# Optimization experiments

Measured on AMD Instinct MI355X. Metric: run time of the kernel, lower is better.

## Reference

```python
import jax, jax.numpy as jnp
import numpy as np

B, T, C = 4, 2048, 1024
H = 16
D = C // H  # 64

def setup_inputs() -> dict:
    key = jax.random.key(0)
    k1, k2, k3, k4, k5 = jax.random.split(key, 5)
    s = 0.02
    return {
        "x": jax.random.normal(k1, (B, T, C), dtype=jnp.float32),
        "Wqkv": jax.random.normal(k2, (C, 3 * C), dtype=jnp.float32) * s,
        "bqkv": jnp.zeros((3 * C,), dtype=jnp.float32),
        "Wout": jax.random.normal(k3, (C, C), dtype=jnp.float32) * s,
        "bout": jnp.zeros((C,), dtype=jnp.float32),
    }

def reference(x, Wqkv, bqkv, Wout, bout):
    b, t, c = x.shape
    scale = D ** -0.5
    qkv = x @ Wqkv + bqkv                      # [B,T,3C]
    qkv = qkv.reshape(b, t, 3, H, D)
    q = qkv[:, :, 0].transpose(0, 2, 1, 3)     # [B,H,T,D]
    k = qkv[:, :, 1].transpose(0, 2, 1, 3)
    v = qkv[:, :, 2].transpose(0, 2, 1, 3)
    att = jnp.einsum('bhqd,bhkd->bhqk', q, k) * scale
    causal = jnp.tril(jnp.ones((t, t), dtype=bool))
    att = jnp.where(causal, att, -jnp.inf)
    att = jax.nn.softmax(att, axis=-1)
    y = jnp.einsum('bhqk,bhkd->bhqd', att, v)  # [B,H,T,D]
    y = y.transpose(0, 2, 1, 3).reshape(b, t, c)
    return y @ Wout + bout
```

## Files before the change

kernel.cpp:

```cpp
#include <hip/hip_runtime.h>
#include <hip/hip_bf16.h>


using f32x4 = __attribute__((ext_vector_type(4))) float;
using s16x8 = __attribute__((ext_vector_type(8))) short;
using s16x4 = __attribute__((ext_vector_type(4))) short;

#define MFMA16(a, b, c) __builtin_amdgcn_mfma_f32_16x16x32_bf16(a, b, c, 0, 0, 0)

__device__ __forceinline__ unsigned short f2bf(float f) {
    unsigned u = __builtin_bit_cast(unsigned, f);
    u += 0x7fffu + ((u >> 16) & 1u);
    return (unsigned short)(u >> 16);
}

__device__ __forceinline__ void gl_lds16(const void* g, void* l) {
    __builtin_amdgcn_global_load_lds(
        (const __attribute__((address_space(1))) void*)g,
        (__attribute__((address_space(3))) void*)l, 16, 0, 0);
}

#define VMCNT(N) asm volatile("s_waitcnt vmcnt(" #N ")" ::: "memory")
#define RBAR()   __builtin_amdgcn_s_barrier()

__global__ __launch_bounds__(256) void cvt_x(const float* __restrict__ x,
                                             unsigned short* __restrict__ xb, int n4) {
    int i = blockIdx.x * 256 + threadIdx.x;
    if (i < n4) {
        f32x4 v = ((const f32x4*)x)[i];
        s16x4 o;
        o[0] = (short)f2bf(v[0]); o[1] = (short)f2bf(v[1]);
        o[2] = (short)f2bf(v[2]); o[3] = (short)f2bf(v[3]);
        ((s16x4*)xb)[i] = o;
    }
}

__global__ __launch_bounds__(256) void cvt_tr(const float* __restrict__ W,
                                              unsigned short* __restrict__ Wt,
                                              int R, int Cc) {
    __shared__ unsigned short tile[64][72];
    const int r0 = blockIdx.x * 64, c0 = blockIdx.y * 64;
    const int tid = threadIdx.x;
    const int r = tid >> 4, c4 = (tid & 15) * 4;
#pragma unroll
    for (int i = 0; i < 4; ++i) {
        f32x4 v = *(const f32x4*)(W + (size_t)(r0 + r + i * 16) * Cc + c0 + c4);
#pragma unroll
        for (int j = 0; j < 4; ++j) tile[r + i * 16][c4 + j] = f2bf(v[j]);
    }
    __syncthreads();
#pragma unroll
    for (int i = 0; i < 4; ++i) {
        s16x4 o;
#pragma unroll
        for (int j = 0; j < 4; ++j) o[j] = (short)tile[c4 + j][r + i * 16];
        *(s16x4*)(Wt + (size_t)(c0 + r + i * 16) * R + r0 + c4) = o;
    }
}

template <int MODE>
__global__ __launch_bounds__(256, 2) void gemm_bt(
    const unsigned short* __restrict__ A, const unsigned short* __restrict__ Bt,
    const float* __restrict__ bias,
    unsigned short* __restrict__ qp, unsigned short* __restrict__ kp,
    unsigned short* __restrict__ vtp, float* __restrict__ outp,
    int M, int N, int K)
{
    __shared__ unsigned short As[2][128 * 64];
    __shared__ unsigned short Bs[2][128 * 64];

    const int tid  = threadIdx.x;
    const int lane = tid & 63, w = tid >> 6;
    const int wm = w >> 1, wn = w & 1;
    const int g = lane >> 4, li = lane & 15;
    const int m0 = blockIdx.x * 128, n0 = blockIdx.y * 128;

    const int srow = lane >> 3;
    const int ssw  = ((lane & 7) ^ srow) * 8;

    f32x4 acc[4][4] = {};

    auto STAGE = [&](int buf, int k0) {
#pragma unroll
        for (int j = 0; j < 4; ++j) {
            const int rr = w * 32 + j * 8;
            gl_lds16(A  + (size_t)(m0 + rr + srow) * K + k0 + ssw, &As[buf][rr * 64]);
            gl_lds16(Bt + (size_t)(n0 + rr + srow) * K + k0 + ssw, &Bs[buf][rr * 64]);
        }
    };

    STAGE(0, 0);
    VMCNT(0);
    __syncthreads();

    const int nt = K >> 6;
    int cur = 0;
    for (int t = 0; t < nt; ++t) {
        if (t + 1 < nt) STAGE(cur ^ 1, (t + 1) << 6);

        s16x8 af[4][2], bf[4][2];
#pragma unroll
        for (int i = 0; i < 4; ++i) {
            const int ra = wm * 64 + i * 16 + li;
            const int rb = wn * 64 + i * 16 + li;
#pragma unroll
            for (int kk = 0; kk < 2; ++kk) {
                af[i][kk] = *(const s16x8*)(
                    &As[cur][ra * 64 + (((kk * 4 + g) ^ (ra & 7)) << 3)]);
                bf[i][kk] = *(const s16x8*)(
                    &Bs[cur][rb * 64 + (((kk * 4 + g) ^ (rb & 7)) << 3)]);
            }
        }

        __builtin_amdgcn_s_setprio(1);
#pragma unroll
        for (int kk = 0; kk < 2; ++kk)
#pragma unroll
            for (int mi = 0; mi < 4; ++mi)
#pragma unroll
                for (int ni = 0; ni < 4; ++ni)
                    acc[mi][ni] = MFMA16(af[mi][kk], bf[ni][kk], acc[mi][ni]);
        __builtin_amdgcn_s_setprio(0);

        VMCNT(0);
        __syncthreads();
        cur ^= 1;
    }

#pragma unroll
    for (int ni = 0; ni < 4; ++ni) {
        const int n = n0 + wn * 64 + ni * 16 + li;
        const float bv = bias[n];
        const int s = n >> 10, h = (n >> 6) & 15, d = n & 63;
#pragma unroll
        for (int mi = 0; mi < 4; ++mi) {
            const int mB = m0 + wm * 64 + mi * 16 + g * 4;
            float v0 = acc[mi][ni][0] + bv, v1 = acc[mi][ni][1] + bv;
            float v2 = acc[mi][ni][2] + bv, v3 = acc[mi][ni][3] + bv;
            if (MODE == 0) {
                const int b = mB >> 11, tt = mB & 2047;
                if (s == 2) {
                    unsigned pk01, pk23;
                    asm("v_cvt_pk_bf16_f32 %0, %1, %2" : "=v"(pk01) : "v"(v0), "v"(v1));
                    asm("v_cvt_pk_bf16_f32 %0, %1, %2" : "=v"(pk23) : "v"(v2), "v"(v3));
                    unsigned short* dst = vtp + ((size_t)(b * 16 + h) * 64 + d) * 2048 + tt;
                    *(unsigned*)dst = pk01;
                    *(unsigned*)(dst + 2) = pk23;
                } else {
                    const float sc2 = (s == 0) ? 0.1803368801111143f : 1.0f;
                    unsigned short* dst =
                        ((s == 0) ? qp : kp) + ((size_t)(b * 16 + h) * 2048 + tt) * 64 + d;
                    dst[0]   = f2bf(v0 * sc2);
                    dst[64]  = f2bf(v1 * sc2);
                    dst[128] = f2bf(v2 * sc2);
                    dst[192] = f2bf(v3 * sc2);
                }
            } else {
                float* dst = outp + (size_t)mB * N + n;
                dst[0] = v0; dst[N] = v1; dst[2 * N] = v2; dst[3 * N] = v3;
            }
        }
    }
}

__device__ __forceinline__ void softmax_pack(
    f32x4 (&sT)[4], f32x4 (&O)[4], float& m, float& l,
    char* PsRow, s16x8& pf0, s16x8& pf1,
    int kbase, int wq0, int qrow, int g, int li)
{
    if (kbase + 63 > wq0) {
#pragma unroll
        for (int nf = 0; nf < 4; ++nf)
#pragma unroll
            for (int r = 0; r < 4; ++r)
                if (kbase + nf * 16 + g * 4 + r > qrow) sT[nf][r] = -1e30f;
    }

    float t0 = fmaxf(fmaxf(sT[0][0], sT[0][1]), sT[0][2]);
    float t1 = fmaxf(fmaxf(sT[0][3], sT[1][0]), sT[1][1]);
    float t2 = fmaxf(fmaxf(sT[1][2], sT[1][3]), sT[2][0]);
    float t3 = fmaxf(fmaxf(sT[2][1], sT[2][2]), sT[2][3]);
    float t4 = fmaxf(fmaxf(sT[3][0], sT[3][1]), sT[3][2]);
    float mx = fmaxf(fmaxf(t0, t1), t2);
    mx = fmaxf(fmaxf(mx, t3), fmaxf(t4, sT[3][3]));
    mx = fmaxf(mx, __shfl_xor(mx, 16));
    mx = fmaxf(mx, __shfl_xor(mx, 32));

    if (__any(mx > m + 8.f)) {
        const float mnew = fmaxf(m, mx);
        const float fac  = __builtin_amdgcn_exp2f(m - mnew);
        m = mnew;
        l *= fac;
        float facr[4];
#pragma unroll
        for (int r = 0; r < 4; ++r) facr[r] = __shfl(fac, g * 4 + r);
#pragma unroll
        for (int nf = 0; nf < 4; ++nf)
#pragma unroll
            for (int r = 0; r < 4; ++r) O[nf][r] *= facr[r];
    }

    float rs = 0.f;
#pragma unroll
    for (int nf = 0; nf < 4; ++nf)
#pragma unroll
        for (int r = 0; r < 4; ++r) {
            float p = __builtin_amdgcn_exp2f(sT[nf][r] - m);
            sT[nf][r] = p;
            rs += p;
        }
    rs += __shfl_xor(rs, 16);
    rs += __shfl_xor(rs, 32);
    l += rs;

    const int swz = (li & 7) << 4;
    char* rowp = PsRow + li * 128;
#pragma unroll
    for (int nf = 0; nf < 4; ++nf) {
        unsigned pk0, pk1;
        asm("v_cvt_pk_bf16_f32 %0, %1, %2" : "=v"(pk0) : "v"(sT[nf][0]), "v"(sT[nf][1]));
        asm("v_cvt_pk_bf16_f32 %0, %1, %2" : "=v"(pk1) : "v"(sT[nf][2]), "v"(sT[nf][3]));
        uint2 pv; pv.x = pk0; pv.y = pk1;
        *(uint2*)(rowp + ((nf * 32 + g * 8) ^ swz)) = pv;
    }
    pf0 = *(const s16x8*)(rowp + ((g * 16) ^ swz));
    pf1 = *(const s16x8*)(rowp + ((64 + g * 16) ^ swz));
}

__global__ __launch_bounds__(256, 4) void attn_k(
    const unsigned short* __restrict__ qbuf,
    const unsigned short* __restrict__ kbuf,
    const unsigned short* __restrict__ vtbuf,
    unsigned short* __restrict__ ybuf)
{
    __shared__ unsigned short Ks[2][4096];
    __shared__ unsigned short Vs[2][4096];
    __shared__ unsigned short Ps[4][16][64];

    const int tid  = threadIdx.x;
    const int lane = tid & 63, w = tid >> 6;
    const int g = lane >> 4, li = lane & 15;

    const int id   = blockIdx.x;
    const int slot = id >> 3;
    const int bh   = (id & 7) * 8 + (slot & 7);
    const int bx   = slot >> 3;
    const int qtA  = 31 - bx, qtB = bx;

    const unsigned short* qb  = qbuf  + (size_t)bh * 131072;
    const unsigned short* kb  = kbuf  + (size_t)bh * 131072;
    const unsigned short* vtb = vtbuf + (size_t)bh * 131072;
    const int b = bh >> 4, h = bh & 15;

    const int srow = lane >> 3;
    const int ssw  = ((lane & 7) ^ srow) * 8;

    auto STAGE = [&](int p, int kbase) {
#pragma unroll
        for (int jj = 0; jj < 2; ++jj) {
            const int j = w * 2 + jj, row = j * 8 + srow;
            gl_lds16(kb  + (size_t)(kbase + row) * 64 + ssw, &Ks[p][j * 512]);
            gl_lds16(vtb + (size_t)row * 2048 + kbase + ssw, &Vs[p][j * 512]);
        }
    };

    const int wqA = qtA * 64 + w * 16, qrowA = wqA + li;
    const int wqB = qtB * 64 + w * 16, qrowB = wqB + li;

    const unsigned short* qrA = qb + (size_t)qrowA * 64 + g * 8;
    const s16x8 qfA0 = *(const s16x8*)qrA;
    const s16x8 qfA1 = *(const s16x8*)(qrA + 32);
    const unsigned short* qrB = qb + (size_t)qrowB * 64 + g * 8;
    const s16x8 qfB0 = *(const s16x8*)qrB;
    const s16x8 qfB1 = *(const s16x8*)(qrB + 32);

    f32x4 OA[4] = {}, OB[4] = {};
    float mA = -1e30f, lA = 0.f, mB = -1e30f, lB = 0.f;

    const int nkb = qtA + 1;
    STAGE(0, 0);

    for (int t = 0; t < nkb; ++t) {
        const int p = t & 1;
        const int kbase = t * 64;
        const bool actB = (t <= qtB);
        const bool more = (t + 1 < nkb);

        if (more) {
            STAGE(p ^ 1, kbase + 64);
            VMCNT(4);
        } else {
            VMCNT(0);
        }
        RBAR();

        f32x4 sA[4], sB[4];
        __builtin_amdgcn_s_setprio(1);
#pragma unroll
        for (int nf = 0; nf < 4; ++nf) {
            const int r = nf * 16 + li;
            const unsigned short* Kp = &Ks[p][r * 64];
            s16x8 kf0 = *(const s16x8*)(Kp + ((g ^ (li & 7)) << 3));
            s16x8 kf1 = *(const s16x8*)(Kp + (((g + 4) ^ (li & 7)) << 3));
            f32x4 a = {};
            a = MFMA16(kf0, qfA0, a);
            a = MFMA16(kf1, qfA1, a);
            sA[nf] = a;
            f32x4 bb = {};
            if (actB) {
                bb = MFMA16(kf0, qfB0, bb);
                bb = MFMA16(kf1, qfB1, bb);
            }
            sB[nf] = bb;
        }
        __builtin_amdgcn_s_setprio(0);

        s16x8 pfA0, pfA1, pfB0, pfB1;
        softmax_pack(sA, OA, mA, lA, (char*)&Ps[w][0][0], pfA0, pfA1,
                     kbase, wqA, qrowA, g, li);
        if (actB)
            softmax_pack(sB, OB, mB, lB, (char*)&Ps[w][0][0], pfB0, pfB1,
                         kbase, wqB, qrowB, g, li);

        __builtin_amdgcn_s_setprio(1);
#pragma unroll
        for (int nf = 0; nf < 4; ++nf) {
            const int d = nf * 16 + li;
            const unsigned short* Vp = &Vs[p][d * 64];
            s16x8 vf0 = *(const s16x8*)(Vp + ((g ^ (li & 7)) << 3));
            s16x8 vf1 = *(const s16x8*)(Vp + (((g + 4) ^ (li & 7)) << 3));
            OA[nf] = MFMA16(pfA0, vf0, OA[nf]);
            OA[nf] = MFMA16(pfA1, vf1, OA[nf]);
            if (actB) {
                OB[nf] = MFMA16(pfB0, vf0, OB[nf]);
                OB[nf] = MFMA16(pfB1, vf1, OB[nf]);
            }
        }
        __builtin_amdgcn_s_setprio(0);

        if (more) RBAR();
    }

    {
        const float linv = __builtin_amdgcn_rcpf(lA);
        float lr[4];
#pragma unroll
        for (int r = 0; r < 4; ++r) lr[r] = __shfl(linv, g * 4 + r);
#pragma unroll
        for (int nf = 0; nf < 4; ++nf)
#pragma unroll
            for (int r = 0; r < 4; ++r) {
                const int row = wqA + g * 4 + r;
                ybuf[((size_t)(b * 2048 + row)) * 1024 + h * 64 + nf * 16 + li] =
                    f2bf(OA[nf][r] * lr[r]);
            }
    }
    {
        const float linv = __builtin_amdgcn_rcpf(lB);
        float lr[4];
#pragma unroll
        for (int r = 0; r < 4; ++r) lr[r] = __shfl(linv, g * 4 + r);
#pragma unroll
        for (int nf = 0; nf < 4; ++nf)
#pragma unroll
            for (int r = 0; r < 4; ++r) {
                const int row = wqB + g * 4 + r;
                ybuf[((size_t)(b * 2048 + row)) * 1024 + h * 64 + nf * 16 + li] =
                    f2bf(OB[nf][r] * lr[r]);
            }
    }
}

extern "C" void kernel_launch(void* const* d_in, const int* in_sizes, int n_in,
                              void* d_out, int out_size, void* d_ws, size_t ws_size,
                              hipStream_t stream)
{
    const float* x    = (const float*)d_in[0];
    const float* Wqkv = (const float*)d_in[1];
    const float* bqkv = (const float*)d_in[2];
    const float* Wout = (const float*)d_in[3];
    const float* bout = (const float*)d_in[4];

    unsigned short* ws0 = (unsigned short*)d_ws;
    unsigned short* ws1 = ws0 + (size_t)8388608;
    unsigned short* ws2 = ws0 + (size_t)2 * 8388608;
    unsigned short* ws3 = ws0 + (size_t)3 * 8388608;

    unsigned short* xbf   = (unsigned short*)d_out;
    unsigned short* WqkvT = xbf + (size_t)8388608;

    cvt_x<<<8192, 256, 0, stream>>>(x, xbf, 2097152);
    cvt_tr<<<dim3(16, 48), 256, 0, stream>>>(Wqkv, WqkvT, 1024, 3072);
    gemm_bt<0><<<dim3(64, 24), 256, 0, stream>>>(
        xbf, WqkvT, bqkv, ws0, ws1, ws2, nullptr, 8192, 3072, 1024);
    attn_k<<<1024, 256, 0, stream>>>(ws0, ws1, ws2, ws3);
    cvt_tr<<<dim3(16, 16), 256, 0, stream>>>(Wout, ws0, 1024, 1024);
    gemm_bt<1><<<dim3(64, 8), 256, 0, stream>>>(
        ws3, ws0, bout, nullptr, nullptr, nullptr, (float*)d_out, 8192, 1024, 1024);
}
```

Baseline: 169.7 us.

## Switch attention to 32x32 MFMA with per-wave tiles and permlane P transpose

Rewrites the attention inner loop to use 32x32x16 bf16 MFMAs. Each wave now owns 32 query rows of one of the two paired tiles, where before every wave handled 16 rows of both tiles. The P matrix is rearranged into operand layout with permlane32_swap instead of a round trip through shared memory, which removes the Ps buffer and its LDS traffic. The cost is load imbalance: waves on the short tile sit idle through most iterations while waves on the long tile do all the work, and the larger accumulators raise register pressure.

```diff
diff --git a/kernel.cpp b/kernel.cpp
--- a/kernel.cpp
+++ b/kernel.cpp
@@ -2,11 +2,13 @@
 #include <hip/hip_bf16.h>
 
 
-using f32x4 = __attribute__((ext_vector_type(4))) float;
-using s16x8 = __attribute__((ext_vector_type(8))) short;
-using s16x4 = __attribute__((ext_vector_type(4))) short;
+using f32x4  = __attribute__((ext_vector_type(4))) float;
+using f32x16 = __attribute__((ext_vector_type(16))) float;
+using s16x8  = __attribute__((ext_vector_type(8))) short;
+using s16x4  = __attribute__((ext_vector_type(4))) short;
 
 #define MFMA16(a, b, c) __builtin_amdgcn_mfma_f32_16x16x32_bf16(a, b, c, 0, 0, 0)
+#define MFMA32(a, b, c) __builtin_amdgcn_mfma_f32_32x32x16_bf16(a, b, c, 0, 0, 0)
 
 __device__ __forceinline__ unsigned short f2bf(float f) {
     unsigned u = __builtin_bit_cast(unsigned, f);
@@ -163,70 +165,6 @@
     }
 }
 
-__device__ __forceinline__ void softmax_pack(
-    f32x4 (&sT)[4], f32x4 (&O)[4], float& m, float& l,
-    char* PsRow, s16x8& pf0, s16x8& pf1,
-    int kbase, int wq0, int qrow, int g, int li)
-{
-    if (kbase + 63 > wq0) {
-#pragma unroll
-        for (int nf = 0; nf < 4; ++nf)
-#pragma unroll
-            for (int r = 0; r < 4; ++r)
-                if (kbase + nf * 16 + g * 4 + r > qrow) sT[nf][r] = -1e30f;
-    }
-
-    float t0 = fmaxf(fmaxf(sT[0][0], sT[0][1]), sT[0][2]);
-    float t1 = fmaxf(fmaxf(sT[0][3], sT[1][0]), sT[1][1]);
-    float t2 = fmaxf(fmaxf(sT[1][2], sT[1][3]), sT[2][0]);
-    float t3 = fmaxf(fmaxf(sT[2][1], sT[2][2]), sT[2][3]);
-    float t4 = fmaxf(fmaxf(sT[3][0], sT[3][1]), sT[3][2]);
-    float mx = fmaxf(fmaxf(t0, t1), t2);
-    mx = fmaxf(fmaxf(mx, t3), fmaxf(t4, sT[3][3]));
-    mx = fmaxf(mx, __shfl_xor(mx, 16));
-    mx = fmaxf(mx, __shfl_xor(mx, 32));
-
-    if (__any(mx > m + 8.f)) {
-        const float mnew = fmaxf(m, mx);
-        const float fac  = __builtin_amdgcn_exp2f(m - mnew);
-        m = mnew;
-        l *= fac;
-        float facr[4];
-#pragma unroll
-        for (int r = 0; r < 4; ++r) facr[r] = __shfl(fac, g * 4 + r);
-#pragma unroll
-        for (int nf = 0; nf < 4; ++nf)
-#pragma unroll
-            for (int r = 0; r < 4; ++r) O[nf][r] *= facr[r];
-    }
-
-    float rs = 0.f;
-#pragma unroll
-    for (int nf = 0; nf < 4; ++nf)
-#pragma unroll
-        for (int r = 0; r < 4; ++r) {
-            float p = __builtin_amdgcn_exp2f(sT[nf][r] - m);
-            sT[nf][r] = p;
-            rs += p;
-        }
-    rs += __shfl_xor(rs, 16);
-    rs += __shfl_xor(rs, 32);
-    l += rs;
-
-    const int swz = (li & 7) << 4;
-    char* rowp = PsRow + li * 128;
-#pragma unroll
-    for (int nf = 0; nf < 4; ++nf) {
-        unsigned pk0, pk1;
-        asm("v_cvt_pk_bf16_f32 %0, %1, %2" : "=v"(pk0) : "v"(sT[nf][0]), "v"(sT[nf][1]));
-        asm("v_cvt_pk_bf16_f32 %0, %1, %2" : "=v"(pk1) : "v"(sT[nf][2]), "v"(sT[nf][3]));
-        uint2 pv; pv.x = pk0; pv.y = pk1;
-        *(uint2*)(rowp + ((nf * 32 + g * 8) ^ swz)) = pv;
-    }
-    pf0 = *(const s16x8*)(rowp + ((g * 16) ^ swz));
-    pf1 = *(const s16x8*)(rowp + ((64 + g * 16) ^ swz));
-}
-
 __global__ __launch_bounds__(256, 4) void attn_k(
     const unsigned short* __restrict__ qbuf,
     const unsigned short* __restrict__ kbuf,
@@ -235,11 +173,11 @@
 {
     __shared__ unsigned short Ks[2][4096];
     __shared__ unsigned short Vs[2][4096];
-    __shared__ unsigned short Ps[4][16][64];
 
     const int tid  = threadIdx.x;
     const int lane = tid & 63, w = tid >> 6;
-    const int g = lane >> 4, li = lane & 15;
+    const int l31 = lane & 31;
+    const int h5  = lane >> 5;
 
     const int id   = blockIdx.x;
     const int slot = id >> 3;
@@ -247,6 +185,9 @@
     const int bx   = slot >> 3;
     const int qtA  = 31 - bx, qtB = bx;
 
+    const int Tw    = (w < 2) ? qtA : qtB;
+    const int wrow0 = Tw * 64 + (w & 1) * 32;
+
     const unsigned short* qb  = qbuf  + (size_t)bh * 131072;
     const unsigned short* kb  = kbuf  + (size_t)bh * 131072;
     const unsigned short* vtb = vtbuf + (size_t)bh * 131072;
@@ -264,18 +205,14 @@
         }
     };
 
-    const int wqA = qtA * 64 + w * 16, qrowA = wqA + li;
-    const int wqB = qtB * 64 + w * 16, qrowB = wqB + li;
-
-    const unsigned short* qrA = qb + (size_t)qrowA * 64 + g * 8;
-    const s16x8 qfA0 = *(const s16x8*)qrA;
-    const s16x8 qfA1 = *(const s16x8*)(qrA + 32);
-    const unsigned short* qrB = qb + (size_t)qrowB * 64 + g * 8;
-    const s16x8 qfB0 = *(const s16x8*)qrB;
-    const s16x8 qfB1 = *(const s16x8*)(qrB + 32);
-
-    f32x4 OA[4] = {}, OB[4] = {};
-    float mA = -1e30f, lA = 0.f, mB = -1e30f, lB = 0.f;
+    const int qrow = wrow0 + l31;
+    const unsigned short* qr = qb + (size_t)qrow * 64 + h5 * 8;
+    s16x8 qf[4];
+#pragma unroll
+    for (int s = 0; s < 4; ++s) qf[s] = *(const s16x8*)(qr + s * 16);
+
+    f32x16 O0 = {}, O1 = {};
+    float m = -1e30f, lsum = 0.f;
 
     const int nkb = qtA + 1;
     STAGE(0, 0);
@@ -283,7 +220,6 @@
     for (int t = 0; t < nkb; ++t) {
         const int p = t & 1;
         const int kbase = t * 64;
-        const bool actB = (t <= qtB);
         const bool more = (t + 1 < nkb);
 
         if (more) {
@@ -294,80 +230,109 @@
         }
         RBAR();
 
-        f32x4 sA[4], sB[4];
-        __builtin_amdgcn_s_setprio(1);
-#pragma unroll
-        for (int nf = 0; nf < 4; ++nf) {
-            const int r = nf * 16 + li;
-            const unsigned short* Kp = &Ks[p][r * 64];
-            s16x8 kf0 = *(const s16x8*)(Kp + ((g ^ (li & 7)) << 3));
-            s16x8 kf1 = *(const s16x8*)(Kp + (((g + 4) ^ (li & 7)) << 3));
-            f32x4 a = {};
-            a = MFMA16(kf0, qfA0, a);
-            a = MFMA16(kf1, qfA1, a);
-            sA[nf] = a;
-            f32x4 bb = {};
-            if (actB) {
-                bb = MFMA16(kf0, qfB0, bb);
-                bb = MFMA16(kf1, qfB1, bb);
-            }
-            sB[nf] = bb;
-        }
-        __builtin_amdgcn_s_setprio(0);
-
-        s16x8 pfA0, pfA1, pfB0, pfB1;
-        softmax_pack(sA, OA, mA, lA, (char*)&Ps[w][0][0], pfA0, pfA1,
-                     kbase, wqA, qrowA, g, li);
-        if (actB)
-            softmax_pack(sB, OB, mB, lB, (char*)&Ps[w][0][0], pfB0, pfB1,
-                         kbase, wqB, qrowB, g, li);
-
-        __builtin_amdgcn_s_setprio(1);
-#pragma unroll
-        for (int nf = 0; nf < 4; ++nf) {
-            const int d = nf * 16 + li;
-            const unsigned short* Vp = &Vs[p][d * 64];
-            s16x8 vf0 = *(const s16x8*)(Vp + ((g ^ (li & 7)) << 3));
-            s16x8 vf1 = *(const s16x8*)(Vp + (((g + 4) ^ (li & 7)) << 3));
-            OA[nf] = MFMA16(pfA0, vf0, OA[nf]);
-            OA[nf] = MFMA16(pfA1, vf1, OA[nf]);
-            if (actB) {
-                OB[nf] = MFMA16(pfB0, vf0, OB[nf]);
-                OB[nf] = MFMA16(pfB1, vf1, OB[nf]);
-            }
-        }
-        __builtin_amdgcn_s_setprio(0);
+        if (t <= Tw) {
+            f32x16 s0 = {}, s1 = {};
+            __builtin_amdgcn_s_setprio(1);
+#pragma unroll
+            for (int s = 0; s < 4; ++s) {
+                const int c = s * 2 + h5;
+                const int sw = (c ^ (l31 & 7)) << 3;
+                s16x8 kf0 = *(const s16x8*)(&Ks[p][l31 * 64 + sw]);
+                s16x8 kf1 = *(const s16x8*)(&Ks[p][(32 + l31) * 64 + sw]);
+                s0 = MFMA32(kf0, qf[s], s0);
+                s1 = MFMA32(kf1, qf[s], s1);
+            }
+            __builtin_amdgcn_s_setprio(0);
+
+            if (kbase + 63 > wrow0) {
+#pragma unroll
+                for (int r = 0; r < 16; ++r) {
+                    const int k0 = kbase + (r & 3) + 8 * (r >> 2) + 4 * h5;
+                    if (k0 > qrow)      s0[r] = -1e30f;
+                    if (k0 + 32 > qrow) s1[r] = -1e30f;
+                }
+            }
+
+            float mx = fmaxf(s0[0], s1[0]);
+#pragma unroll
+            for (int r = 1; r < 16; ++r) mx = fmaxf(mx, fmaxf(s0[r], s1[r]));
+            mx = fmaxf(mx, __shfl_xor(mx, 32));
+
+            if (__any(mx > m + 8.f)) {
+                const float mnew = fmaxf(m, mx);
+                const float fac  = __builtin_amdgcn_exp2f(m - mnew);
+                m = mnew;
+                lsum *= fac;
+#pragma unroll
+                for (int r = 0; r < 16; ++r) {
+                    const float fr = __shfl(fac, (r & 3) + 8 * (r >> 2) + 4 * h5);
+                    O0[r] *= fr;
+                    O1[r] *= fr;
+                }
+            }
+
+            float rs = 0.f;
+#pragma unroll
+            for (int r = 0; r < 16; ++r) {
+                s0[r] = __builtin_amdgcn_exp2f(s0[r] - m);
+                s1[r] = __builtin_amdgcn_exp2f(s1[r] - m);
+                rs += s0[r] + s1[r];
+            }
+            rs += __shfl_xor(rs, 32);
+            lsum += rs;
+
+            s16x8 pa[4];
+#pragma unroll
+            for (int G = 0; G < 2; ++G) {
+#pragma unroll
+                for (int half = 0; half < 2; ++half) {
+                    const int bse = half * 8;
+                    unsigned w0, w1, w2, w3;
+                    if (G == 0) {
+                        asm("v_cvt_pk_bf16_f32 %0, %1, %2" : "=v"(w0) : "v"(s0[bse + 0]), "v"(s0[bse + 1]));
+                        asm("v_cvt_pk_bf16_f32 %0, %1, %2" : "=v"(w1) : "v"(s0[bse + 2]), "v"(s0[bse + 3]));
+                        asm("v_cvt_pk_bf16_f32 %0, %1, %2" : "=v"(w2) : "v"(s0[bse + 4]), "v"(s0[bse + 5]));
+                        asm("v_cvt_pk_bf16_f32 %0, %1, %2" : "=v"(w3) : "v"(s0[bse + 6]), "v"(s0[bse + 7]));
+                    } else {
+                        asm("v_cvt_pk_bf16_f32 %0, %1, %2" : "=v"(w0) : "v"(s1[bse + 0]), "v"(s1[bse + 1]));
+                        asm("v_cvt_pk_bf16_f32 %0, %1, %2" : "=v"(w1) : "v"(s1[bse + 2]), "v"(s1[bse + 3]));
+                        asm("v_cvt_pk_bf16_f32 %0, %1, %2" : "=v"(w2) : "v"(s1[bse + 4]), "v"(s1[bse + 5]));
+                        asm("v_cvt_pk_bf16_f32 %0, %1, %2" : "=v"(w3) : "v"(s1[bse + 6]), "v"(s1[bse + 7]));
+                    }
+                    auto r02 = __builtin_amdgcn_permlane32_swap(w0, w2, false, false);
+                    auto r13 = __builtin_amdgcn_permlane32_swap(w1, w3, false, false);
+                    union { unsigned u[4]; s16x8 v; } P;
+                    P.u[0] = r02[0]; P.u[1] = r13[0];
+                    P.u[2] = r02[1]; P.u[3] = r13[1];
+                    pa[G * 2 + half] = P.v;
+                }
+            }
+
+            __builtin_amdgcn_s_setprio(1);
+#pragma unroll
+            for (int kg = 0; kg < 4; ++kg) {
+                const int c = kg * 2 + h5;
+                const int sw = (c ^ (l31 & 7)) << 3;
+                s16x8 vf0 = *(const s16x8*)(&Vs[p][l31 * 64 + sw]);
+                s16x8 vf1 = *(const s16x8*)(&Vs[p][(32 + l31) * 64 + sw]);
+                O0 = MFMA32(pa[kg], vf0, O0);
+                O1 = MFMA32(pa[kg], vf1, O1);
+            }
+            __builtin_amdgcn_s_setprio(0);
+        }
 
         if (more) RBAR();
     }
 
-    {
-        const float linv = __builtin_amdgcn_rcpf(lA);
-        float lr[4];
-#pragma unroll
-        for (int r = 0; r < 4; ++r) lr[r] = __shfl(linv, g * 4 + r);
-#pragma unroll
-        for (int nf = 0; nf < 4; ++nf)
-#pragma unroll
-            for (int r = 0; r < 4; ++r) {
-                const int row = wqA + g * 4 + r;
-                ybuf[((size_t)(b * 2048 + row)) * 1024 + h * 64 + nf * 16 + li] =
-                    f2bf(OA[nf][r] * lr[r]);
-            }
-    }
-    {
-        const float linv = __builtin_amdgcn_rcpf(lB);
-        float lr[4];
-#pragma unroll
-        for (int r = 0; r < 4; ++r) lr[r] = __shfl(linv, g * 4 + r);
-#pragma unroll
-        for (int nf = 0; nf < 4; ++nf)
-#pragma unroll
-            for (int r = 0; r < 4; ++r) {
-                const int row = wqB + g * 4 + r;
-                ybuf[((size_t)(b * 2048 + row)) * 1024 + h * 64 + nf * 16 + li] =
-                    f2bf(OB[nf][r] * lr[r]);
-            }
+    const float linv = __builtin_amdgcn_rcpf(lsum);
+#pragma unroll
+    for (int r = 0; r < 16; ++r) {
+        const int qi = (r & 3) + 8 * (r >> 2) + 4 * h5;
+        const float lr = __shfl(linv, qi);
+        const int row = wrow0 + qi;
+        const size_t base = ((size_t)(b * 2048 + row)) * 1024 + h * 64;
+        ybuf[base + l31]      = f2bf(O0[r] * lr);
+        ybuf[base + 32 + l31] = f2bf(O1[r] * lr);
     }
 }
 
```

Measured after the change: 173.8 us. +2.4%, slower.
